# Optimization experiments

Hardware: AMD Instinct MI355X
Metric: run time of the kernel (lower is better)

## Reference

```python
import jax, jax.numpy as jnp
import numpy as np

B, N, E = 16, 1024, 256
H, D = 16, 16            # head_num * qkv_dim == embedding_dim
FF = 2 * E               # ff_size = embedding_dim * 2
EPS = 1e-5


def setup_inputs() -> dict:
    key = jax.random.key(0)
    ks = jax.random.split(key, 12)
    s = lambda fan_in: 1.0 / np.sqrt(fan_in)
    return {
        "x":  jax.random.normal(ks[0], (B, N, E), dtype=jnp.float32),
        # attention projections (nn.Linear, bias=False) stored as [in, out]
        "Wq": jax.random.uniform(ks[1], (E, H * D), jnp.float32, -s(E), s(E)),
        "Wk": jax.random.uniform(ks[2], (E, H * D), jnp.float32, -s(E), s(E)),
        "Wv": jax.random.uniform(ks[3], (E, H * D), jnp.float32, -s(E), s(E)),
        "Wo": jax.random.uniform(ks[4], (H * D, E), jnp.float32, -s(H * D), s(H * D)),
        "bo": jax.random.uniform(ks[5], (E,), jnp.float32, -s(H * D), s(H * D)),
        # InstanceNorm1d affine params
        "gamma1": jnp.ones((E,), jnp.float32),
        "beta1":  jnp.zeros((E,), jnp.float32),
        "gamma2": jnp.ones((E,), jnp.float32),
        "beta2":  jnp.zeros((E,), jnp.float32),
        # SwiGLU FFN: Linear(E, 2*FF) -> SwiGLU -> Linear(FF, E)
        "W1": jax.random.uniform(ks[6], (E, 2 * FF), jnp.float32, -s(E), s(E)),
        "b1": jax.random.uniform(ks[7], (2 * FF,), jnp.float32, -s(E), s(E)),
        "W2": jax.random.uniform(ks[8], (FF, E), jnp.float32, -s(FF), s(FF)),
        "b2": jax.random.uniform(ks[9], (E,), jnp.float32, -s(FF), s(FF)),
    }


def _instance_norm(x, gamma, beta):
    # x: [B, N, E]; normalize over N per (batch, channel), biased variance
    mean = jnp.mean(x, axis=1, keepdims=True)
    var = jnp.mean(jnp.square(x - mean), axis=1, keepdims=True)
    return (x - mean) * jax.lax.rsqrt(var + EPS) * gamma + beta


def reference(x, Wq, Wk, Wv, Wo, bo, gamma1, beta1, gamma2, beta2, W1, b1, W2, b2):
    b, n, e = x.shape
    q = (x @ Wq).reshape(b, n, H, D)
    k = (x @ Wk).reshape(b, n, H, D)
    v = (x @ Wv).reshape(b, n, H, D)
    scores = jnp.einsum("bnhd,bmhd->bhnm", q, k) / np.sqrt(D)   # [B,H,N,N]
    weights = jax.nn.softmax(scores, axis=-1)
    attn = jnp.einsum("bhnm,bmhd->bnhd", weights, v).reshape(b, n, H * D)
    mha = attn @ Wo + bo
    h = _instance_norm(mha + x, gamma1, beta1)
    # SwiGLU FFN: chunk -> (x_part, gate); silu(gate) * x_part
    proj = h @ W1 + b1
    x_part, gate = proj[..., :FF], proj[..., FF:]
    ff = (jax.nn.silu(gate) * x_part) @ W2 + b2
    return _instance_norm(h + ff, gamma2, beta2)
```

## Files before the change

kernel.cpp:

```cpp
#include <hip/hip_runtime.h>
#include <stdint.h>

typedef unsigned short u16;
typedef __bf16 bf16x8 __attribute__((ext_vector_type(8)));
typedef float f32x4 __attribute__((ext_vector_type(4)));

__device__ __forceinline__ float bf2f(u16 v){ return __uint_as_float(((unsigned)v)<<16); }
__device__ __forceinline__ u16 f2bf(float f){
  unsigned u = __float_as_uint(f);
  unsigned r = (u + 0x7FFFu + ((u>>16)&1u)) >> 16;
  return (u16)r;
}
__device__ __forceinline__ float fexp2(float x){
#if __has_builtin(__builtin_amdgcn_exp2f)
  return __builtin_amdgcn_exp2f(x);
#else
  return exp2f(x);
#endif
}

__global__ void prep_kernel(const float* __restrict__ x_, u16* __restrict__ xb,
                            const float* __restrict__ Wq, const float* __restrict__ Wk,
                            const float* __restrict__ Wv, const float* __restrict__ Wo,
                            const float* __restrict__ W1, const float* __restrict__ W2,
                            u16* __restrict__ wqkvT, u16* __restrict__ woT,
                            u16* __restrict__ w1T, u16* __restrict__ w2T,
                            float* __restrict__ SS)
{
  int bid = blockIdx.x;
  int t = threadIdx.x;
  if (bid >= 640) {
    int idx = ((bid - 640) * 256 + t) * 8;
    float4 a0 = *(const float4*)(x_ + idx);
    float4 a1 = *(const float4*)(x_ + idx + 4);
    union { u16 u[8]; uint4 v; } pk;
    pk.u[0] = f2bf(a0.x); pk.u[1] = f2bf(a0.y); pk.u[2] = f2bf(a0.z); pk.u[3] = f2bf(a0.w);
    pk.u[4] = f2bf(a1.x); pk.u[5] = f2bf(a1.y); pk.u[6] = f2bf(a1.z); pk.u[7] = f2bf(a1.w);
    *(uint4*)(xb + idx) = pk.v;
    return;
  }
  if (bid < 64) SS[bid * 256 + t] = 0.f;
  __shared__ u16 tile[32][33];
  const float* in; u16* out; int K, N, t2; bool glu = false;
  if (bid < 64)       { in = Wq; out = wqkvT;           K = 256; N = 256;  t2 = bid; }
  else if (bid < 128) { in = Wk; out = wqkvT + 65536;   K = 256; N = 256;  t2 = bid - 64; }
  else if (bid < 192) { in = Wv; out = wqkvT + 131072;  K = 256; N = 256;  t2 = bid - 128; }
  else if (bid < 256) { in = Wo; out = woT;             K = 256; N = 256;  t2 = bid - 192; }
  else if (bid < 512) { in = W1; out = w1T;             K = 256; N = 1024; t2 = bid - 256; glu = true; }
  else                { in = W2; out = w2T;             K = 512; N = 256;  t2 = bid - 512; }
  int ntn = N >> 5;
  int k0 = (t2 / ntn) * 32, n0 = (t2 % ntn) * 32;
  #pragma unroll
  for (int p = 0; p < 4; ++p) {
    int u = t + p * 256; int r = u >> 5, c = u & 31;
    tile[r][c] = f2bf(in[(size_t)(k0 + r) * N + n0 + c]);
  }
  __syncthreads();
  #pragma unroll
  for (int p = 0; p < 4; ++p) {
    int u = t + p * 256; int r = u >> 5, c = u & 31;
    int q = n0 + r;
    int row = glu ? (q < 512 ? 2 * q : 2 * (q - 512) + 1) : q;
    out[(size_t)row * K + k0 + c] = tile[c][r];
  }
}

enum { MODE_QKV = 0, MODE_Y_RES = 1, MODE_GLU = 2 };

template<int MODE, int TN, int RESN, int STATS, int NORMA>
__launch_bounds__(256, 3)
__global__ void gemm_kernel(const u16* __restrict__ A, const u16* __restrict__ BT,
                            int M, int N, int K,
                            const float* __restrict__ bias, const u16* __restrict__ resp,
                            u16* __restrict__ outB,
                            float* __restrict__ ssum, float* __restrict__ ssq,
                            const float* __restrict__ nsum, const float* __restrict__ nsq,
                            const float* __restrict__ ngam, const float* __restrict__ nbet)
{
  constexpr int NJ = TN / 32;
  __shared__ u16 As[128 * 40];
  __shared__ u16 Bs[TN * 40];
  __shared__ float scA[256], sfA[256];
  const int t = threadIdx.x;
  const int m0 = blockIdx.x * 128;
  const int n0 = blockIdx.y * TN;
  const int lane = t & 63;
  const int w = t >> 6;
  const int wm = (w >> 1) * 64;
  const int wn = (w & 1) * (NJ * 16);
  const int fr = lane & 15;
  const int fg = lane >> 4;
  const int bIdx = m0 >> 10;
  const float inv1024 = 1.f / 1024.f;

  if (NORMA) {
    int e = t;
    float mean = nsum[bIdx * 256 + e] * inv1024;
    float var = nsq[bIdx * 256 + e] * inv1024 - mean * mean;
    float rstd = rsqrtf(var + 1e-5f);
    float sc = rstd * ngam[e];
    scA[e] = sc;
    sfA[e] = nbet[e] - mean * sc;
  }

  f32x4 acc[4][NJ];
  #pragma unroll
  for (int i = 0; i < 4; ++i)
    #pragma unroll
    for (int j = 0; j < NJ; ++j)
      acc[i][j] = (f32x4){0.f, 0.f, 0.f, 0.f};

  constexpr int TOT = (128 + TN) * 4;
  for (int k0 = 0; k0 < K; k0 += 32) {
    __syncthreads();
    #pragma unroll
    for (int u = 0; u < TOT / 256; ++u) {
      int uu = t + u * 256;
      if (uu < 512) {
        int row = uu >> 2, cb = uu & 3;
        if (NORMA) {
          union { u16 u[8]; uint4 v; } in, o;
          in.v = *(const uint4*)(A + (size_t)(m0 + row) * K + k0 + cb * 8);
          const float* scp = scA + k0 + cb * 8;
          const float* sfp = sfA + k0 + cb * 8;
          float4 s0 = *(const float4*)scp, s1 = *(const float4*)(scp + 4);
          float4 f0 = *(const float4*)sfp, f1 = *(const float4*)(sfp + 4);
          o.u[0] = f2bf(bf2f(in.u[0]) * s0.x + f0.x);
          o.u[1] = f2bf(bf2f(in.u[1]) * s0.y + f0.y);
          o.u[2] = f2bf(bf2f(in.u[2]) * s0.z + f0.z);
          o.u[3] = f2bf(bf2f(in.u[3]) * s0.w + f0.w);
          o.u[4] = f2bf(bf2f(in.u[4]) * s1.x + f1.x);
          o.u[5] = f2bf(bf2f(in.u[5]) * s1.y + f1.y);
          o.u[6] = f2bf(bf2f(in.u[6]) * s1.z + f1.z);
          o.u[7] = f2bf(bf2f(in.u[7]) * s1.w + f1.w);
          *(uint4*)(As + row * 40 + cb * 8) = o.v;
        } else {
          float4 va = *(const float4*)(A + (size_t)(m0 + row) * K + k0 + cb * 8);
          *(float4*)(As + row * 40 + cb * 8) = va;
        }
      } else {
        int v2 = uu - 512;
        int row = v2 >> 2, cb = v2 & 3;
        float4 vb = *(const float4*)(BT + (size_t)(n0 + row) * K + k0 + cb * 8);
        *(float4*)(Bs + row * 40 + cb * 8) = vb;
      }
    }
    __syncthreads();
    bf16x8 af[4], bfr[NJ];
    #pragma unroll
    for (int i = 0; i < 4; ++i) af[i]  = *(const bf16x8*)(As + (wm + i * 16 + fr) * 40 + fg * 8);
    #pragma unroll
    for (int j = 0; j < NJ; ++j) bfr[j] = *(const bf16x8*)(Bs + (wn + j * 16 + fr) * 40 + fg * 8);
    #pragma unroll
    for (int i = 0; i < 4; ++i)
      #pragma unroll
      for (int j = 0; j < NJ; ++j)
        acc[i][j] = __builtin_amdgcn_mfma_f32_16x16x32_bf16(af[i], bfr[j], acc[i][j], 0, 0, 0);
  }

  #pragma unroll
  for (int j = 0; j < NJ; ++j) {
    int col = n0 + wn + j * 16 + fr;
    float bv = 0.f;
    if (MODE == MODE_Y_RES) bv = bias[col];
    if (MODE == MODE_GLU)   bv = bias[(col >> 1) + ((col & 1) << 9)];
    float scj = 0.f, sfj = 0.f;
    if (RESN == 2) {
      float mean = nsum[bIdx * 256 + col] * inv1024;
      float var = nsq[bIdx * 256 + col] * inv1024 - mean * mean;
      float rstd = rsqrtf(var + 1e-5f);
      scj = rstd * ngam[col];
      sfj = nbet[col] - mean * scj;
    }
    float sj = 0.f, qj = 0.f;
    #pragma unroll
    for (int i = 0; i < 4; ++i) {
      #pragma unroll
      for (int r = 0; r < 4; ++r) {
        int row = m0 + wm + i * 16 + fg * 4 + r;
        float v = acc[i][j][r] + bv;
        if (MODE == MODE_QKV) {
          int which = col >> 8, h = (col >> 4) & 15, d = col & 15;
          int b = row >> 10, ns = row & 1023;
          outB[(size_t)which * 4194304 + (((size_t)(b * 16 + h) * 1024 + ns) * 16 + d)] = f2bf(v);
        } else if (MODE == MODE_Y_RES) {
          size_t idx = (size_t)row * N + col;
          float rv = bf2f(resp[idx]);
          if (RESN == 2) rv = rv * scj + sfj;
          float y = v + rv;
          outB[idx] = f2bf(y);
          if (STATS) { sj += y; qj += y * y; }
        } else {
          float partner = __shfl_xor(v, 1);
          if ((fr & 1) == 0) {
            float g = partner / (1.f + __expf(-partner));
            outB[(size_t)row * 512 + (col >> 1)] = f2bf(g * v);
          }
        }
      }
    }
    if (STATS) {
      sj += __shfl_xor(sj, 16); sj += __shfl_xor(sj, 32);
      qj += __shfl_xor(qj, 16); qj += __shfl_xor(qj, 32);
      if (fg == 0) {
        atomicAdd(&ssum[bIdx * 256 + col], sj);
        atomicAdd(&ssq[bIdx * 256 + col], qj);
      }
    }
  }
}

#define SCALE_L2 0.360673760222241f

__launch_bounds__(512, 4)
__global__ void attn_kernel(const u16* __restrict__ Q, const u16* __restrict__ Kg,
                            const u16* __restrict__ Vg, u16* __restrict__ attn)
{
  __shared__ u16 Ks[2][128 * 24];
  __shared__ u16 Vt[2][16 * 136];
  __shared__ u16 Pb[8][16 * 40];
  const int t = threadIdx.x;
  const int bh = blockIdx.x & 255;
  const int qg = blockIdx.x >> 8;
  const int b = bh >> 4, h = bh & 15;
  const size_t base = (size_t)bh * 16384;
  const int w = t >> 6, lane = t & 63;
  const int fr = lane & 15, fg = lane >> 4;
  u16* Pw = Pb[w];
  const int q0 = qg * 128 + w * 16;
  const f32x4 zero4 = (f32x4){0.f, 0.f, 0.f, 0.f};

  const int su = (t & 255) >> 1;
  const int sh = t & 1;
  const bool isK = t < 256;
  const int blk = su >> 5, ii = su & 31;
  const int kpos = blk * 32 + ((ii & 1) ? 16 + (ii >> 1) : (ii >> 1));

  bf16x8 qf = {};
  if (fg < 2) {
    union { u16 u[8]; uint4 v; bf16x8 f; } qt;
    qt.v = *(const uint4*)(Q + base + (size_t)(q0 + fr) * 16 + fg * 8);
    #pragma unroll
    for (int j = 0; j < 8; ++j) qt.u[j] = f2bf(bf2f(qt.u[j]) * SCALE_L2);
    qf = qt.f;
  }

  {
    uint4 pre = isK ? *(const uint4*)(Kg + base + (size_t)su * 16 + sh * 8)
                    : *(const uint4*)(Vg + base + (size_t)su * 16 + sh * 8);
    if (isK) {
      *(uint4*)(&Ks[0][kpos * 24 + sh * 8]) = pre;
    } else {
      union { u16 u[8]; uint4 v; } pk; pk.v = pre;
      #pragma unroll
      for (int j = 0; j < 8; ++j) Vt[0][(sh * 8 + j) * 136 + su] = pk.u[j];
    }
  }
  __syncthreads();

  f32x4 acco = zero4;
  float lsum[4] = {0.f, 0.f, 0.f, 0.f};

  for (int c = 0; c < 8; ++c) {
    uint4 nxt;
    if (c < 7) {
      const size_t off = base + (size_t)((c + 1) * 128 + su) * 16 + sh * 8;
      nxt = isK ? *(const uint4*)(Kg + off) : *(const uint4*)(Vg + off);
    }
    const u16* KsC = Ks[c & 1];
    const u16* VtC = Vt[c & 1];
    #pragma unroll
    for (int sub = 0; sub < 4; ++sub) {
      const int kb = sub * 32;
      bf16x8 kf0 = {}, kf1 = {};
      if (fg < 2) {
        kf0 = *(const bf16x8*)(KsC + (kb + fr) * 24 + fg * 8);
        kf1 = *(const bf16x8*)(KsC + (kb + 16 + fr) * 24 + fg * 8);
      }
      f32x4 s0 = __builtin_amdgcn_mfma_f32_16x16x32_bf16(qf, kf0, zero4, 0, 0, 0);
      f32x4 s1 = __builtin_amdgcn_mfma_f32_16x16x32_bf16(qf, kf1, zero4, 0, 0, 0);
      #pragma unroll
      for (int r = 0; r < 4; ++r) {
        float p0 = fexp2(s0[r]);
        float p1 = fexp2(s1[r]);
        lsum[r] += p0 + p1;
        *(unsigned*)(Pw + (fg * 4 + r) * 40 + 2 * fr) =
            __builtin_amdgcn_perm(__float_as_uint(p1), __float_as_uint(p0), 0x07060302u);
      }
      __asm__ volatile("s_waitcnt lgkmcnt(0)" ::: "memory");
      bf16x8 pf = *(const bf16x8*)(Pw + fr * 40 + fg * 8);
      bf16x8 vf = *(const bf16x8*)(VtC + fr * 136 + kb + fg * 8);
      __asm__ volatile("" ::: "memory");
      acco = __builtin_amdgcn_mfma_f32_16x16x32_bf16(pf, vf, acco, 0, 0, 0);
    }
    if (c < 7) {
      if (isK) {
        *(uint4*)(&Ks[(c + 1) & 1][kpos * 24 + sh * 8]) = nxt;
      } else {
        union { u16 u[8]; uint4 v; } pk; pk.v = nxt;
        #pragma unroll
        for (int j = 0; j < 8; ++j) Vt[(c + 1) & 1][(sh * 8 + j) * 136 + su] = pk.u[j];
      }
    }
    __syncthreads();
  }

  #pragma unroll
  for (int r = 0; r < 4; ++r) {
    float l = lsum[r];
    l += __shfl_xor(l, 1); l += __shfl_xor(l, 2);
    l += __shfl_xor(l, 4); l += __shfl_xor(l, 8);
    int row = q0 + fg * 4 + r;
    attn[((size_t)(b * 1024 + row)) * 256 + h * 16 + fr] = f2bf(acco[r] / l);
  }
}

__global__ void apply_kernel(const u16* __restrict__ y, const float* __restrict__ ssum,
                             const float* __restrict__ ssq, const float* __restrict__ gamma,
                             const float* __restrict__ beta, float* __restrict__ outp)
{
  int idx = (blockIdx.x * 256 + threadIdx.x) * 4;
  int e = idx & 255;
  int b = idx >> 18;
  union { u16 u[4]; uint2 v; } in;
  in.v = *(const uint2*)(y + idx);
  float ov[4];
  const float inv = 1.f / 1024.f;
  #pragma unroll
  for (int j = 0; j < 4; ++j) {
    int ej = e + j;
    float mean = ssum[b * 256 + ej] * inv;
    float var = ssq[b * 256 + ej] * inv - mean * mean;
    float rstd = rsqrtf(var + 1e-5f);
    ov[j] = (bf2f(in.u[j]) - mean) * rstd * gamma[ej] + beta[ej];
  }
  *(float4*)(outp + idx) = make_float4(ov[0], ov[1], ov[2], ov[3]);
}

extern "C" void kernel_launch(void* const* d_in, const int* in_sizes, int n_in,
                              void* d_out, int out_size, void* d_ws, size_t ws_size,
                              hipStream_t stream)
{
  const float* x      = (const float*)d_in[0];
  const float* Wq     = (const float*)d_in[1];
  const float* Wk     = (const float*)d_in[2];
  const float* Wv     = (const float*)d_in[3];
  const float* Wo     = (const float*)d_in[4];
  const float* bo     = (const float*)d_in[5];
  const float* gamma1 = (const float*)d_in[6];
  const float* beta1  = (const float*)d_in[7];
  const float* gamma2 = (const float*)d_in[8];
  const float* beta2  = (const float*)d_in[9];
  const float* W1     = (const float*)d_in[10];
  const float* b1     = (const float*)d_in[11];
  const float* W2     = (const float*)d_in[12];
  const float* b2     = (const float*)d_in[13];

  char* ws = (char*)d_ws;
  u16*   WQKVT = (u16*)(ws + 0);
  u16*   WOT   = (u16*)(ws + 393216);
  u16*   W1T   = (u16*)(ws + 524288);
  u16*   W2T   = (u16*)(ws + 1048576);
  float* SS    = (float*)(ws + 1310720);
  float* SSUM1 = SS;
  float* SSQ1  = SS + 4096;
  float* SSUM2 = SS + 8192;
  float* SSQ2  = SS + 12288;
  u16*   xb    = (u16*)(ws + 1376256);
  u16*   Qb    = (u16*)(ws + 9764864);
  u16*   ATTN  = (u16*)(ws + 34930688);
  u16*   Y1    = (u16*)(ws + 9764864);
  u16*   G     = (u16*)(ws + 18153472);
  u16*   Y2    = (u16*)(ws + 34930688);

  prep_kernel<<<2688, 256, 0, stream>>>(x, xb, Wq, Wk, Wv, Wo, W1, W2,
                                        WQKVT, WOT, W1T, W2T, SS);

  gemm_kernel<MODE_QKV, 128, 0, 0, 0><<<dim3(128, 6), 256, 0, stream>>>(
      xb, WQKVT, 16384, 768, 256, nullptr, nullptr, Qb,
      nullptr, nullptr, nullptr, nullptr, nullptr, nullptr);

  attn_kernel<<<2048, 512, 0, stream>>>(Qb, Qb + 4194304, Qb + 8388608, ATTN);

  gemm_kernel<MODE_Y_RES, 64, 1, 1, 0><<<dim3(128, 4), 256, 0, stream>>>(
      ATTN, WOT, 16384, 256, 256, bo, xb, Y1,
      SSUM1, SSQ1, nullptr, nullptr, nullptr, nullptr);

  gemm_kernel<MODE_GLU, 128, 0, 0, 1><<<dim3(128, 8), 256, 0, stream>>>(
      Y1, W1T, 16384, 1024, 256, b1, nullptr, G,
      nullptr, nullptr, SSUM1, SSQ1, gamma1, beta1);

  gemm_kernel<MODE_Y_RES, 64, 2, 1, 0><<<dim3(128, 4), 256, 0, stream>>>(
      G, W2T, 16384, 256, 512, b2, Y1, Y2,
      SSUM2, SSQ2, SSUM1, SSQ1, gamma1, beta1);

  apply_kernel<<<4096, 256, 0, stream>>>(Y2, SSUM2, SSQ2, gamma2, beta2, (float*)d_out);
}
```

Measured before the change: 225.9 us.

## Prefetch GEMM tiles into registers with BK=64 and stage epilogue through LDS

The GEMM kernel now loads the next K-slice (64 wide instead of 32) into registers while MFMAs run on the current LDS tile, halving barrier count and hiding global latency. The epilogue writes results to a shared-memory tile and then emits 16-byte coalesced stores for QKV, residual and GLU outputs instead of scattered 2-byte stores. The cost is a larger LDS footprint and more prefetch registers, which may reduce occupancy under the launch bound of 3 blocks. GLU now rounds x and gate to bf16 before SiLU, which slightly changes numerics.

```diff
diff --git a/kernel.cpp b/kernel.cpp
--- a/kernel.cpp
+++ b/kernel.cpp
@@ -78,8 +78,13 @@
                             const float* __restrict__ ngam, const float* __restrict__ nbet)
 {
   constexpr int NJ = TN / 32;
-  __shared__ u16 As[128 * 40];
-  __shared__ u16 Bs[TN * 40];
+  constexpr int AU = 4;
+  constexpr int BU = TN / 32;
+  constexpr int STG = (128 + TN) * 72;
+  constexpr int TSZ = 128 * (TN + 8);
+  __shared__ u16 LDSbuf[STG > TSZ ? STG : TSZ];
+  u16* As = LDSbuf;
+  u16* Bs = LDSbuf + 128 * 72;
   __shared__ float scA[256], sfA[256];
   const int t = threadIdx.x;
   const int m0 = blockIdx.x * 128;
@@ -110,57 +115,71 @@
     for (int j = 0; j < NJ; ++j)
       acc[i][j] = (f32x4){0.f, 0.f, 0.f, 0.f};
 
-  constexpr int TOT = (128 + TN) * 4;
-  for (int k0 = 0; k0 < K; k0 += 32) {
+  const int arow = t >> 3, acb = t & 7;
+  uint4 ra[AU], rb[BU];
+  #pragma unroll
+  for (int u = 0; u < AU; ++u)
+    ra[u] = *(const uint4*)(A + (size_t)(m0 + arow + u * 32) * K + acb * 8);
+  #pragma unroll
+  for (int u = 0; u < BU; ++u)
+    rb[u] = *(const uint4*)(BT + (size_t)(n0 + arow + u * 32) * K + acb * 8);
+
+  const int NS = K >> 6;
+  for (int s = 0; s < NS; ++s) {
     __syncthreads();
     #pragma unroll
-    for (int u = 0; u < TOT / 256; ++u) {
-      int uu = t + u * 256;
-      if (uu < 512) {
-        int row = uu >> 2, cb = uu & 3;
-        if (NORMA) {
-          union { u16 u[8]; uint4 v; } in, o;
-          in.v = *(const uint4*)(A + (size_t)(m0 + row) * K + k0 + cb * 8);
-          const float* scp = scA + k0 + cb * 8;
-          const float* sfp = sfA + k0 + cb * 8;
-          float4 s0 = *(const float4*)scp, s1 = *(const float4*)(scp + 4);
-          float4 f0 = *(const float4*)sfp, f1 = *(const float4*)(sfp + 4);
-          o.u[0] = f2bf(bf2f(in.u[0]) * s0.x + f0.x);
-          o.u[1] = f2bf(bf2f(in.u[1]) * s0.y + f0.y);
-          o.u[2] = f2bf(bf2f(in.u[2]) * s0.z + f0.z);
-          o.u[3] = f2bf(bf2f(in.u[3]) * s0.w + f0.w);
-          o.u[4] = f2bf(bf2f(in.u[4]) * s1.x + f1.x);
-          o.u[5] = f2bf(bf2f(in.u[5]) * s1.y + f1.y);
-          o.u[6] = f2bf(bf2f(in.u[6]) * s1.z + f1.z);
-          o.u[7] = f2bf(bf2f(in.u[7]) * s1.w + f1.w);
-          *(uint4*)(As + row * 40 + cb * 8) = o.v;
-        } else {
-          float4 va = *(const float4*)(A + (size_t)(m0 + row) * K + k0 + cb * 8);
-          *(float4*)(As + row * 40 + cb * 8) = va;
-        }
+    for (int u = 0; u < AU; ++u) {
+      int row = arow + u * 32;
+      if (NORMA) {
+        union { u16 u[8]; uint4 v; } in, o;
+        in.v = ra[u];
+        int kb = s * 64 + acb * 8;
+        const float* scp = scA + kb;
+        const float* sfp = sfA + kb;
+        #pragma unroll
+        for (int q = 0; q < 8; ++q) o.u[q] = f2bf(bf2f(in.u[q]) * scp[q] + sfp[q]);
+        *(uint4*)(As + row * 72 + acb * 8) = o.v;
       } else {
-        int v2 = uu - 512;
-        int row = v2 >> 2, cb = v2 & 3;
-        float4 vb = *(const float4*)(BT + (size_t)(n0 + row) * K + k0 + cb * 8);
-        *(float4*)(Bs + row * 40 + cb * 8) = vb;
-      }
-    }
+        *(uint4*)(As + row * 72 + acb * 8) = ra[u];
+      }
+    }
+    #pragma unroll
+    for (int u = 0; u < BU; ++u)
+      *(uint4*)(Bs + (arow + u * 32) * 72 + acb * 8) = rb[u];
     __syncthreads();
-    bf16x8 af[4], bfr[NJ];
-    #pragma unroll
-    for (int i = 0; i < 4; ++i) af[i]  = *(const bf16x8*)(As + (wm + i * 16 + fr) * 40 + fg * 8);
-    #pragma unroll
-    for (int j = 0; j < NJ; ++j) bfr[j] = *(const bf16x8*)(Bs + (wn + j * 16 + fr) * 40 + fg * 8);
-    #pragma unroll
-    for (int i = 0; i < 4; ++i)
+    if (s + 1 < NS) {
+      int k0 = (s + 1) * 64;
+      #pragma unroll
+      for (int u = 0; u < AU; ++u)
+        ra[u] = *(const uint4*)(A + (size_t)(m0 + arow + u * 32) * K + k0 + acb * 8);
+      #pragma unroll
+      for (int u = 0; u < BU; ++u)
+        rb[u] = *(const uint4*)(BT + (size_t)(n0 + arow + u * 32) * K + k0 + acb * 8);
+    }
+    #pragma unroll
+    for (int kh = 0; kh < 2; ++kh) {
+      bf16x8 af[4], bfr[NJ];
+      #pragma unroll
+      for (int i = 0; i < 4; ++i)
+        af[i] = *(const bf16x8*)(As + (wm + i * 16 + fr) * 72 + kh * 32 + fg * 8);
       #pragma unroll
       for (int j = 0; j < NJ; ++j)
-        acc[i][j] = __builtin_amdgcn_mfma_f32_16x16x32_bf16(af[i], bfr[j], acc[i][j], 0, 0, 0);
-  }
-
+        bfr[j] = *(const bf16x8*)(Bs + (wn + j * 16 + fr) * 72 + kh * 32 + fg * 8);
+      #pragma unroll
+      for (int i = 0; i < 4; ++i)
+        #pragma unroll
+        for (int j = 0; j < NJ; ++j)
+          acc[i][j] = __builtin_amdgcn_mfma_f32_16x16x32_bf16(af[i], bfr[j], acc[i][j], 0, 0, 0);
+    }
+  }
+
+  __syncthreads();
+  u16* Ts = LDSbuf;
+  constexpr int TP = TN + 8;
   #pragma unroll
   for (int j = 0; j < NJ; ++j) {
     int col = n0 + wn + j * 16 + fr;
+    int lcol = wn + j * 16 + fr;
     float bv = 0.f;
     if (MODE == MODE_Y_RES) bv = bias[col];
     if (MODE == MODE_GLU)   bv = bias[(col >> 1) + ((col & 1) << 9)];
@@ -177,26 +196,16 @@
     for (int i = 0; i < 4; ++i) {
       #pragma unroll
       for (int r = 0; r < 4; ++r) {
-        int row = m0 + wm + i * 16 + fg * 4 + r;
+        int lrow = wm + i * 16 + fg * 4 + r;
         float v = acc[i][j][r] + bv;
-        if (MODE == MODE_QKV) {
-          int which = col >> 8, h = (col >> 4) & 15, d = col & 15;
-          int b = row >> 10, ns = row & 1023;
-          outB[(size_t)which * 4194304 + (((size_t)(b * 16 + h) * 1024 + ns) * 16 + d)] = f2bf(v);
-        } else if (MODE == MODE_Y_RES) {
-          size_t idx = (size_t)row * N + col;
+        if (MODE == MODE_Y_RES) {
+          size_t idx = (size_t)(m0 + lrow) * N + col;
           float rv = bf2f(resp[idx]);
           if (RESN == 2) rv = rv * scj + sfj;
-          float y = v + rv;
-          outB[idx] = f2bf(y);
-          if (STATS) { sj += y; qj += y * y; }
-        } else {
-          float partner = __shfl_xor(v, 1);
-          if ((fr & 1) == 0) {
-            float g = partner / (1.f + __expf(-partner));
-            outB[(size_t)row * 512 + (col >> 1)] = f2bf(g * v);
-          }
+          v += rv;
+          if (STATS) { sj += v; qj += v * v; }
         }
+        Ts[lrow * TP + lcol] = f2bf(v);
       }
     }
     if (STATS) {
@@ -206,6 +215,50 @@
         atomicAdd(&ssum[bIdx * 256 + col], sj);
         atomicAdd(&ssq[bIdx * 256 + col], qj);
       }
+    }
+  }
+  __syncthreads();
+
+  if (MODE == MODE_QKV) {
+    #pragma unroll
+    for (int p = 0; p < 8; ++p) {
+      int g = t + p * 256;
+      int lrow = g >> 4, oct = g & 15;
+      int row = m0 + lrow;
+      int col0 = n0 + oct * 8;
+      int which = col0 >> 8, h = (col0 >> 4) & 15, dh = (col0 >> 3) & 1;
+      int b = row >> 10, ns = row & 1023;
+      uint4 v = *(const uint4*)(Ts + lrow * TP + oct * 8);
+      *(uint4*)(outB + (size_t)which * 4194304 +
+                (((size_t)(b * 16 + h) * 1024 + ns) * 16 + dh * 8)) = v;
+    }
+  } else if (MODE == MODE_Y_RES) {
+    #pragma unroll
+    for (int p = 0; p < TN / 16; ++p) {
+      int g = t + p * 256;
+      int lrow = g >> 3, oct = g & 7;
+      uint4 v = *(const uint4*)(Ts + lrow * TP + oct * 8);
+      *(uint4*)(outB + (size_t)(m0 + lrow) * N + n0 + oct * 8) = v;
+    }
+  } else {
+    #pragma unroll
+    for (int p = 0; p < 4; ++p) {
+      int g = t + p * 256;
+      int lrow = g >> 3, grp = g & 7;
+      union { u16 u[8]; uint4 v; } r0, r1, o;
+      r0.v = *(const uint4*)(Ts + lrow * TP + grp * 16);
+      r1.v = *(const uint4*)(Ts + lrow * TP + grp * 16 + 8);
+      #pragma unroll
+      for (int q = 0; q < 4; ++q) {
+        float xv = bf2f(r0.u[2 * q]), gv = bf2f(r0.u[2 * q + 1]);
+        o.u[q] = f2bf(xv * gv / (1.f + __expf(-gv)));
+      }
+      #pragma unroll
+      for (int q = 0; q < 4; ++q) {
+        float xv = bf2f(r1.u[2 * q]), gv = bf2f(r1.u[2 * q + 1]);
+        o.u[4 + q] = f2bf(xv * gv / (1.f + __expf(-gv)));
+      }
+      *(uint4*)(outB + (size_t)(m0 + lrow) * (N >> 1) + (n0 >> 1) + grp * 8) = o.v;
     }
   }
 }
```

Result: slower. 277.9 us (+23.0%).
